# Optimization experiments

Measured on AMD Instinct MI355X. Metric: run time of the kernel, lower is better.

Reference implementation:

```python
import jax, jax.numpy as jnp
import numpy as np

EMBED = 1024
HEADS = 16
HEAD_DIM = EMBED // HEADS
T = 1024
B = 2
TEMP = 1.0
EPS = 1e-20


def setup_inputs() -> dict:
    key = jax.random.key(0)
    ks = jax.random.split(key, 8)
    s = 0.02  # xavier-ish init scale
    return {
        "g": jax.random.normal(ks[0], (T, B, EMBED), dtype=jnp.float32),
        "h": jax.random.normal(ks[1], (T, B, EMBED), dtype=jnp.float32),
        "g_in_w": jax.random.normal(ks[2], (3 * EMBED, EMBED), dtype=jnp.float32) * s,
        "g_in_b": jnp.zeros((3 * EMBED,), dtype=jnp.float32),
        "h_in_w": jax.random.normal(ks[3], (2 * EMBED, EMBED), dtype=jnp.float32) * s,
        "h_in_b": jnp.zeros((2 * EMBED,), dtype=jnp.float32),
        "g_out_w": jax.random.normal(ks[4], (EMBED, EMBED), dtype=jnp.float32) * s,
        "g_out_b": jnp.zeros((EMBED,), dtype=jnp.float32),
        "h_out_w": jax.random.normal(ks[5], (EMBED, EMBED), dtype=jnp.float32) * s,
        "h_out_b": jnp.zeros((EMBED,), dtype=jnp.float32),
    }


def reference(g, h, g_in_w, g_in_b, h_in_w, h_in_b, g_out_w, g_out_b, h_out_w, h_out_b):
    Tt, Bb, E = g.shape
    H, d = HEADS, HEAD_DIM

    # fused qkv projection on g stream, kv on h stream (F.linear: x @ W^T + b)
    q, gk, gv = jnp.split(g @ g_in_w.T + g_in_b, 3, axis=-1)
    hk, hv = jnp.split(h @ h_in_w.T + h_in_b, 2, axis=-1)
    q = q * (d ** -0.5)

    def to_heads(x):  # [T,B,E] -> [B,H,T,d]
        return x.reshape(Tt, Bb, H, d).transpose(1, 2, 0, 3)

    q, gk, gv, hk, hv = map(to_heads, (q, gk, gv, hk, hv))

    # dual-stream attention scores
    g_scores = jnp.einsum("bhtd,bhsd->bhts", q, gk)
    h_scores = jnp.einsum("bhtd,bhsd->bhts", q, hk)

    g_p = jax.nn.softmax(g_scores, axis=-1)
    h_p = jax.nn.softmax(h_scores, axis=-1)

    # gumbel-softmax sample of h_scores (mode='gumbel', temperature=TEMP)
    u = jax.random.uniform(jax.random.key(42), h_scores.shape, dtype=h_scores.dtype)
    noise = -jnp.log(-jnp.log(u + EPS) + EPS)
    sample = jax.nn.softmax((jax.nn.log_softmax(h_scores, axis=-1) + noise) / TEMP, axis=-1)

    g_attn = jnp.einsum("bhts,bhsd->bhtd", g_p, gv)
    h_attn = jnp.einsum("bhts,bhsd->bhtd", sample, hv)

    def merge(x):  # [B,H,T,d] -> [T,B,E]
        return x.transpose(2, 0, 1, 3).reshape(Tt, Bb, E)

    g_out = merge(g_attn) @ g_out_w.T + g_out_b
    h_out = merge(h_attn) @ h_out_w.T + h_out_b
    return g_out, h_out
```

## Files before the change

kernel.cpp:

```cpp
#include <hip/hip_runtime.h>
#include <stdint.h>

#define T_SEQ 1024

typedef __attribute__((ext_vector_type(8))) short short8;
typedef __attribute__((ext_vector_type(4))) float f32x4;
typedef __attribute__((ext_vector_type(4))) unsigned short ushort4v;
typedef __attribute__((ext_vector_type(8))) unsigned short ushort8v;

__device__ __forceinline__ unsigned short f2bf(float f) {
  union { float f; uint32_t u; } v; v.f = f;
  return (unsigned short)((v.u + 0x7fffu + ((v.u >> 16) & 1u)) >> 16);
}
__device__ __forceinline__ float bf2f(unsigned short u) {
  union { uint32_t u; float f; } v; v.u = ((uint32_t)u) << 16;
  return v.f;
}

__device__ __forceinline__ void gl2lds16(const unsigned short* g, unsigned short* l) {
  __builtin_amdgcn_global_load_lds(
      (const __attribute__((address_space(1))) void*)g,
      (__attribute__((address_space(3))) void*)l, 16, 0, 0);
}

__device__ __forceinline__ uint32_t tf_bits(uint32_t flat) {
  const uint32_t ks1 = 42u;
  const uint32_t ks2 = 0x1BD11BDAu ^ 42u;
  uint32_t x0 = 0u;
  uint32_t x1 = flat + ks1;
#define TFR(r) { x0 += x1; x1 = (x1 << (r)) | (x1 >> (32 - (r))); x1 ^= x0; }
  TFR(13) TFR(15) TFR(26) TFR(6)
  x0 += ks1; x1 += ks2 + 1u;
  TFR(17) TFR(29) TFR(16) TFR(24)
  x0 += ks2; x1 += 2u;
  TFR(13) TFR(15) TFR(26) TFR(6)
  x1 += ks1 + 3u;
  TFR(17) TFR(29) TFR(16) TFR(24)
  x0 += ks1; x1 += ks2 + 4u;
  TFR(13) TFR(15) TFR(26) TFR(6)
  x0 += ks2; x1 += 5u;
#undef TFR
  return x0 ^ x1;
}

__device__ __forceinline__ float gumbel_noise(uint32_t flat) {
  const uint32_t bits = tf_bits(flat);
  const float u = __uint_as_float((bits >> 9) | 0x3f800000u) - 1.0f;
  return -__logf(-__logf(u + 1e-20f) + 1e-20f);
}

__global__ __launch_bounds__(256) void convert_pre(
    const float* __restrict__ g, const float* __restrict__ h,
    const float* __restrict__ wgi_f, const float* __restrict__ whi_f,
    const float* __restrict__ wgo_f, const float* __restrict__ who_f,
    unsigned short* __restrict__ gbf, unsigned short* __restrict__ hbf,
    unsigned short* __restrict__ wgi, unsigned short* __restrict__ whi,
    unsigned short* __restrict__ wgo, unsigned short* __restrict__ who)
{
  const int64_t Q_SPLIT = 1048576;
  const int64_t Q_TOTAL = Q_SPLIT + 1835008;
  for (int64_t qd = (int64_t)blockIdx.x * 256 + threadIdx.x; qd < Q_TOTAL;
       qd += (int64_t)gridDim.x * 256) {
    if (qd < Q_SPLIT) {
      const int which = qd >= 524288;
      const int64_t e = (qd - (which ? 524288 : 0)) * 4;
      const float4 v = *(const float4*)((which ? h : g) + e);
      ushort4v u = {f2bf(v.x), f2bf(v.y), f2bf(v.z), f2bf(v.w)};
      *(ushort4v*)((which ? hbf : gbf) + e) = u;
    } else {
      int64_t off = qd - Q_SPLIT;
      const float* src; unsigned short* dst;
      if (off < 786432)                 { src = wgi_f; dst = wgi; }
      else if (off < 1310720)           { off -= 786432;  src = whi_f; dst = whi; }
      else if (off < 1572864)           { off -= 1310720; src = wgo_f; dst = wgo; }
      else                              { off -= 1572864; src = who_f; dst = who; }
      const int64_t e = off * 4;
      const float4 v = *(const float4*)(src + e);
      ushort4v u = {f2bf(v.x), f2bf(v.y), f2bf(v.z), f2bf(v.w)};
      *(ushort4v*)(dst + e) = u;
    }
  }
}

template<int TM, bool BF16OUT>
__device__ __forceinline__ void gemm_plain_core(
    const unsigned short* __restrict__ Ab, const unsigned short* __restrict__ Wb,
    const float* __restrict__ bias, int N, int K, int m0, int n0,
    int scale_limit, void* Cout, unsigned short* sA, unsigned short* sW)
{
  const int tid = threadIdx.x;
  const int w = tid >> 6;
  const int lane = tid & 63;
  const int txl = lane & 15, q = lane >> 4;
  const int wr = (w >> 1) * (TM * 16);
  const int wc = (w & 1) << 6;
  const int lr = lane >> 3, lu = lane & 7;
  const int rx7 = txl & 7;

  const unsigned short* Asrc = Ab + (size_t)(m0 + w * 8 * TM + lr) * K + ((lu ^ lr) << 3);
  const unsigned short* Wsrc = Wb + (size_t)(n0 + w * 32 + lr) * K + ((lu ^ lr) << 3);
  unsigned short* sAd = sA + (w * 8 * TM) * 64;
  unsigned short* sWd = sW + (w * 32) * 64;

  f32x4 acc[TM][4];
#pragma unroll
  for (int i = 0; i < TM; i++)
#pragma unroll
    for (int j = 0; j < 4; j++) acc[i][j] = (f32x4){0.f, 0.f, 0.f, 0.f};

  for (int k0 = 0; k0 < K; k0 += 64) {
    __syncthreads();
#pragma unroll
    for (int i = 0; i < TM; i++)
      gl2lds16(Asrc + (size_t)(8 * i) * K + k0, sAd + (8 * i) * 64);
#pragma unroll
    for (int i = 0; i < 4; i++)
      gl2lds16(Wsrc + (size_t)(8 * i) * K + k0, sWd + (8 * i) * 64);
    __syncthreads();
#pragma unroll
    for (int kk = 0; kk < 2; kk++) {
      const int uoff = ((4 * kk + q) ^ rx7) << 3;
      short8 af[TM], wf[4];
#pragma unroll
      for (int i = 0; i < TM; i++)
        af[i] = *(const short8*)&sA[(wr + 16 * i + txl) * 64 + uoff];
#pragma unroll
      for (int j = 0; j < 4; j++)
        wf[j] = *(const short8*)&sW[(wc + 16 * j + txl) * 64 + uoff];
#pragma unroll
      for (int i = 0; i < TM; i++)
#pragma unroll
        for (int j = 0; j < 4; j++)
          acc[i][j] = __builtin_amdgcn_mfma_f32_16x16x32_bf16(af[i], wf[j], acc[i][j], 0, 0, 0);
    }
  }

#pragma unroll
  for (int j = 0; j < 4; j++) {
    const int col = n0 + wc + 16 * j + txl;
    const float bj = bias[col];
    const float sc = (col < scale_limit) ? 0.125f : 1.0f;
#pragma unroll
    for (int i = 0; i < TM; i++) {
      const int rbase = m0 + wr + 16 * i + 4 * q;
#pragma unroll
      for (int r = 0; r < 4; r++) {
        const float v = (acc[i][j][r] + bj) * sc;
        if (BF16OUT) ((unsigned short*)Cout)[(size_t)(rbase + r) * N + col] = f2bf(v);
        else         ((float*)Cout)[(size_t)(rbase + r) * N + col] = v;
      }
    }
  }
}

__global__ __launch_bounds__(256, 4) void gemm_inproj(
    const unsigned short* __restrict__ gbf, const unsigned short* __restrict__ wgi,
    const float* __restrict__ bgi,
    const unsigned short* __restrict__ hbf, const unsigned short* __restrict__ whi,
    const float* __restrict__ bhi,
    unsigned short* __restrict__ qkv, unsigned short* __restrict__ hkv)
{
  __shared__ __align__(16) unsigned short sm[16384];
  const int bx = blockIdx.x;
  const int m0 = blockIdx.y * 128;
  if (bx < 24)
    gemm_plain_core<4, true>(gbf, wgi, bgi, 3072, 1024, m0, bx * 128, 1024,
                             qkv, sm, sm + 8192);
  else
    gemm_plain_core<4, true>(hbf, whi, bhi, 2048, 1024, m0, (bx - 24) * 128, 0,
                             hkv, sm, sm + 8192);
}

__global__ __launch_bounds__(256, 2) void gemm_outproj(
    const unsigned short* __restrict__ attnb,
    const unsigned short* __restrict__ wgo, const float* __restrict__ bgo,
    const unsigned short* __restrict__ who, const float* __restrict__ bho,
    float* __restrict__ out)
{
  __shared__ __align__(16) unsigned short sm[12288];
  const int m0 = blockIdx.y * 64;
  const unsigned short* Wp = (m0 < 2048) ? wgo : who;
  const float* bp = (m0 < 2048) ? bgo : bho;
  gemm_plain_core<2, false>(attnb, Wp, bp, 1024, 1024, m0, blockIdx.x * 128, 0,
                            out, sm, sm + 4096);
}

__global__ __launch_bounds__(256) void transpose_v(
    const unsigned short* __restrict__ qkv, const unsigned short* __restrict__ hkv,
    unsigned short* __restrict__ vTg, unsigned short* __restrict__ vTh)
{
  __shared__ __align__(16) unsigned short sm[64 * 72];
  const int tid = threadIdx.x;
  const int t0 = blockIdx.x * 64;
  const int d0 = blockIdx.y * 64;
  const int zb = blockIdx.z;
  const int b = zb & 1;
  const int strm = zb >> 1;
  const unsigned short* src = strm ? hkv : qkv;
  const int srcoff = strm ? 1024 : 2048;
  const int sstride = strm ? 2048 : 3072;
  unsigned short* dst = strm ? vTh : vTg;

  const int r = tid >> 2, cs = (tid & 3) << 4;
  {
    const size_t gsrc = (size_t)((t0 + r) * 2 + b) * sstride + srcoff + d0 + cs;
    *(ushort8v*)&sm[r * 72 + cs]     = *(const ushort8v*)&src[gsrc];
    *(ushort8v*)&sm[r * 72 + cs + 8] = *(const ushort8v*)&src[gsrc + 8];
  }
  __syncthreads();
  const int dr = tid >> 2, ts = (tid & 3) << 4;
  ushort8v o0, o1;
#pragma unroll
  for (int m = 0; m < 8; m++) o0[m] = sm[(ts + m) * 72 + dr];
#pragma unroll
  for (int m = 0; m < 8; m++) o1[m] = sm[(ts + 8 + m) * 72 + dr];
  const size_t gdst = (size_t)b * 1048576 + (size_t)(d0 + dr) * 1024 + t0 + ts;
  *(ushort8v*)&dst[gdst]     = o0;
  *(ushort8v*)&dst[gdst + 8] = o1;
}

__global__ __launch_bounds__(256, 4) void attn_mfma(
    const unsigned short* __restrict__ qkv, const unsigned short* __restrict__ hkv,
    const unsigned short* __restrict__ vTg, const unsigned short* __restrict__ vTh,
    float* __restrict__ Opart, float* __restrict__ lpart)
{
  __shared__ __align__(16) unsigned short smem[17408];
  unsigned short* KV = smem;
  unsigned short* PC = smem + 8192;
  unsigned short* QS = smem + 8192;

  const int tid = threadIdx.x;
  const int w = tid >> 6;
  const int lane = tid & 63;
  const int txl = lane & 15, q = lane >> 4;
  const int rx7 = txl & 7;
  const int lr = lane >> 3, lu = lane & 7;
  const int su = (lu ^ lr) << 3;
  const int t0 = blockIdx.x * 64;
  const int bh = blockIdx.y;
  const int z = blockIdx.z;
  const int b = bh >> 4;
  const int head = bh & 15;
  const int hoff = head * 64;
  const int sr = tid >> 2;
  const int sc = (tid & 3) << 4;

  {
    const size_t gq = ((size_t)(t0 + sr) * 2 + b) * 3072 + hoff + sc;
    *(ushort8v*)&QS[sr * 72 + sc]     = *(const ushort8v*)&qkv[gq];
    *(ushort8v*)&QS[sr * 72 + sc + 8] = *(const ushort8v*)&qkv[gq + 8];
  }
  __syncthreads();
  const short8 aq0 = *(const short8*)&QS[(16 * w + txl) * 72 + 8 * q];
  const short8 aq1 = *(const short8*)&QS[(16 * w + txl) * 72 + 32 + 8 * q];

  f32x4 Og[4], Oh[4];
  float l_g[4], l_h[4];
#pragma unroll
  for (int i = 0; i < 4; i++) {
    Og[i] = (f32x4){0.f, 0.f, 0.f, 0.f};
    Oh[i] = (f32x4){0.f, 0.f, 0.f, 0.f};
    l_g[i] = 0.f; l_h[i] = 0.f;
  }

  unsigned short* pcg = PC + (w * 2 + 0) * 1152;
  unsigned short* pch = PC + (w * 2 + 1) * 1152;

  const int s_begin = z * (T_SEQ / 2);
  const int s_end = s_begin + (T_SEQ / 2);
  for (int s0 = s_begin; s0 < s_end; s0 += 64) {
    __syncthreads();
#pragma unroll
    for (int t = 0; t < 2; t++) {
      const int srow = w * 16 + t * 8 + lr;
      const size_t grow = (size_t)(s0 + srow) * 2 + b;
      gl2lds16(&qkv[grow * 3072 + 1024 + hoff + su], &KV[(w * 16 + t * 8) * 64]);
      gl2lds16(&hkv[grow * 2048 +        hoff + su], &KV[4096 + (w * 16 + t * 8) * 64]);
    }
    float ng[4][4];
#pragma unroll
    for (int nt = 0; nt < 4; nt++)
#pragma unroll
      for (int r = 0; r < 4; r++) {
        const uint32_t trow = (uint32_t)(t0 + 16 * w + 4 * q + r);
        const uint32_t scol_ = (uint32_t)(s0 + 16 * nt + txl);
        ng[nt][r] = gumbel_noise(((uint32_t)bh << 20) | (trow << 10) | scol_);
      }
    __syncthreads();

    f32x4 Sg[4], Sh[4];
    const f32x4 zz = (f32x4){0.f, 0.f, 0.f, 0.f};
#pragma unroll
    for (int nt = 0; nt < 4; nt++) {
      const int srw = (16 * nt + txl) * 64;
      const int u0 = (q ^ rx7) << 3;
      const int u1 = ((4 + q) ^ rx7) << 3;
      const short8 bg0 = *(const short8*)&KV[srw + u0];
      const short8 bg1 = *(const short8*)&KV[srw + u1];
      const short8 bh0 = *(const short8*)&KV[4096 + srw + u0];
      const short8 bh1 = *(const short8*)&KV[4096 + srw + u1];
      f32x4 ag = __builtin_amdgcn_mfma_f32_16x16x32_bf16(aq0, bg0, zz, 0, 0, 0);
      ag = __builtin_amdgcn_mfma_f32_16x16x32_bf16(aq1, bg1, ag, 0, 0, 0);
      f32x4 ah = __builtin_amdgcn_mfma_f32_16x16x32_bf16(aq0, bh0, zz, 0, 0, 0);
      ah = __builtin_amdgcn_mfma_f32_16x16x32_bf16(aq1, bh1, ah, 0, 0, 0);
      Sg[nt] = ag; Sh[nt] = ah;
    }

#pragma unroll
    for (int nt = 0; nt < 4; nt++) {
      float eg[4], eh[4];
#pragma unroll
      for (int r = 0; r < 4; r++) {
        eg[r] = __expf(Sg[nt][r]);            l_g[r] += eg[r];
        eh[r] = __expf(Sh[nt][r] + ng[nt][r]); l_h[r] += eh[r];
      }
      const int sbase = (16 * nt + txl) * 18 + 4 * q;
      *(uint32_t*)&pcg[sbase]     = (uint32_t)f2bf(eg[0]) | ((uint32_t)f2bf(eg[1]) << 16);
      *(uint32_t*)&pcg[sbase + 2] = (uint32_t)f2bf(eg[2]) | ((uint32_t)f2bf(eg[3]) << 16);
      *(uint32_t*)&pch[sbase]     = (uint32_t)f2bf(eh[0]) | ((uint32_t)f2bf(eh[1]) << 16);
      *(uint32_t*)&pch[sbase + 2] = (uint32_t)f2bf(eh[2]) | ((uint32_t)f2bf(eh[3]) << 16);
    }

    __syncthreads();
#pragma unroll
    for (int t = 0; t < 2; t++) {
      const int drow = w * 16 + t * 8 + lr;
      const size_t gv = (size_t)b * 1048576 + (size_t)(hoff + drow) * 1024 + s0 + su;
      gl2lds16(&vTg[gv], &KV[(w * 16 + t * 8) * 64]);
      gl2lds16(&vTh[gv], &KV[4096 + (w * 16 + t * 8) * 64]);
    }
    short8 apg[2], aph[2];
#pragma unroll
    for (int c = 0; c < 2; c++)
#pragma unroll
      for (int j = 0; j < 8; j++) {
        apg[c][j] = (short)pcg[(32 * c + 8 * q + j) * 18 + txl];
        aph[c][j] = (short)pch[(32 * c + 8 * q + j) * 18 + txl];
      }
    __syncthreads();

#pragma unroll
    for (int c = 0; c < 2; c++) {
#pragma unroll
      for (int nt = 0; nt < 4; nt++) {
        const int drw = (16 * nt + txl) * 64;
        const int uv = (((4 * c + q) ^ rx7)) << 3;
        const short8 bvg = *(const short8*)&KV[drw + uv];
        const short8 bvh = *(const short8*)&KV[4096 + drw + uv];
        Og[nt] = __builtin_amdgcn_mfma_f32_16x16x32_bf16(apg[c], bvg, Og[nt], 0, 0, 0);
        Oh[nt] = __builtin_amdgcn_mfma_f32_16x16x32_bf16(aph[c], bvh, Oh[nt], 0, 0, 0);
      }
    }
  }

  float* opg = Opart + ((size_t)(z * 2 + 0) * 2048) * 1024;
  float* oph = Opart + ((size_t)(z * 2 + 1) * 2048) * 1024;
  float* lpg = lpart + (size_t)(z * 2 + 0) * 2048 * 16;
  float* lph = lpart + (size_t)(z * 2 + 1) * 2048 * 16;
#pragma unroll
  for (int r = 0; r < 4; r++) {
    float lg = l_g[r], lh = l_h[r];
    lg += __shfl_xor(lg, 1); lg += __shfl_xor(lg, 2);
    lg += __shfl_xor(lg, 4); lg += __shfl_xor(lg, 8);
    lh += __shfl_xor(lh, 1); lh += __shfl_xor(lh, 2);
    lh += __shfl_xor(lh, 4); lh += __shfl_xor(lh, 8);
    const int row = (t0 + 16 * w + 4 * q + r) * 2 + b;
    if (txl == 0) {
      lpg[row * 16 + head] = lg;
      lph[row * 16 + head] = lh;
    }
    const size_t base = (size_t)row * 1024 + hoff;
#pragma unroll
    for (int nt = 0; nt < 4; nt++) {
      opg[base + 16 * nt + txl] = Og[nt][r];
      oph[base + 16 * nt + txl] = Oh[nt][r];
    }
  }
}

__global__ __launch_bounds__(256) void merge_attn(
    const float* __restrict__ Opart, const float* __restrict__ lpart,
    unsigned short* __restrict__ attnb)
{
  const int idx = blockIdx.x * 256 + threadIdx.x;
  const int st = idx >> 19;
  const int i = idx & 0x7FFFF;
  const int row = i >> 8;
  const int colq = i & 255;
  const int head = colq >> 4;
  const float4 o0 = *(const float4*)&Opart[((size_t)(0 + st) * 2048 + row) * 1024 + colq * 4];
  const float4 o1 = *(const float4*)&Opart[((size_t)(2 + st) * 2048 + row) * 1024 + colq * 4];
  const float l0 = lpart[(size_t)(0 + st) * 32768 + row * 16 + head];
  const float l1 = lpart[(size_t)(2 + st) * 32768 + row * 16 + head];
  const float inv = 1.0f / (l0 + l1);
  ushort4v u = {f2bf((o0.x + o1.x) * inv), f2bf((o0.y + o1.y) * inv),
                f2bf((o0.z + o1.z) * inv), f2bf((o0.w + o1.w) * inv)};
  *(ushort4v*)&attnb[((size_t)st * 2048 + row) * 1024 + colq * 4] = u;
}

extern "C" void kernel_launch(void* const* d_in, const int* in_sizes, int n_in,
                              void* d_out, int out_size, void* d_ws, size_t ws_size,
                              hipStream_t stream) {
  const float* g       = (const float*)d_in[0];
  const float* h       = (const float*)d_in[1];
  const float* g_in_w  = (const float*)d_in[2];
  const float* g_in_b  = (const float*)d_in[3];
  const float* h_in_w  = (const float*)d_in[4];
  const float* h_in_b  = (const float*)d_in[5];
  const float* g_out_w = (const float*)d_in[6];
  const float* g_out_b = (const float*)d_in[7];
  const float* h_out_w = (const float*)d_in[8];
  const float* h_out_b = (const float*)d_in[9];
  float* out = (float*)d_out;

  unsigned short* ws = (unsigned short*)d_ws;
  unsigned short* qkv   = ws;
  unsigned short* hkv   = qkv + (size_t)2048*3072;
  unsigned short* attnb = hkv + (size_t)2048*2048;
  unsigned short* wgo   = attnb + (size_t)4096*1024;
  unsigned short* who   = wgo + (size_t)1024*1024;
  unsigned short* scratch = who + (size_t)1024*1024;
  unsigned short* gbf = scratch;
  unsigned short* hbf = gbf + (size_t)2048*1024;
  unsigned short* wgi = hbf + (size_t)2048*1024;
  unsigned short* whi = wgi + (size_t)3072*1024;
  float* Opart = (float*)scratch;
  float* lpart = Opart + (size_t)4*2048*1024;
  unsigned short* vTg = (unsigned short*)(lpart + (size_t)4*2048*16);
  unsigned short* vTh = vTg + (size_t)2*1024*1024;

  convert_pre<<<1024, 256, 0, stream>>>(g, h, g_in_w, h_in_w, g_out_w, h_out_w,
                                        gbf, hbf, wgi, whi, wgo, who);
  gemm_inproj<<<dim3(40, 16), 256, 0, stream>>>(
      gbf, wgi, g_in_b, hbf, whi, h_in_b, qkv, hkv);
  transpose_v<<<dim3(16, 16, 4), 256, 0, stream>>>(qkv, hkv, vTg, vTh);
  attn_mfma<<<dim3(T_SEQ / 64, 32, 2), 256, 0, stream>>>(qkv, hkv, vTg, vTh, Opart, lpart);
  merge_attn<<<4096, 256, 0, stream>>>(Opart, lpart, attnb);
  gemm_outproj<<<dim3(8, 64), 256, 0, stream>>>(
      attnb, wgo, g_out_b, who, h_out_b, out);
}
```

Before: 278.1 us.

## Shrink attention key tile to 32, load K and V together, raise occupancy

```diff
diff --git a/kernel.cpp b/kernel.cpp
--- a/kernel.cpp
+++ b/kernel.cpp
@@ -219,15 +219,16 @@
   *(ushort8v*)&dst[gdst + 8] = o1;
 }
 
-__global__ __launch_bounds__(256, 4) void attn_mfma(
+__global__ __launch_bounds__(256, 6) void attn_mfma(
     const unsigned short* __restrict__ qkv, const unsigned short* __restrict__ hkv,
     const unsigned short* __restrict__ vTg, const unsigned short* __restrict__ vTh,
     float* __restrict__ Opart, float* __restrict__ lpart)
 {
-  __shared__ __align__(16) unsigned short smem[17408];
-  unsigned short* KV = smem;
+  __shared__ __align__(16) unsigned short smem[12800];
+  unsigned short* KB = smem;
+  unsigned short* VB = smem + 4096;
   unsigned short* PC = smem + 8192;
-  unsigned short* QS = smem + 8192;
+  unsigned short* QS = smem;
 
   const int tid = threadIdx.x;
   const int w = tid >> 6;
@@ -236,6 +237,8 @@
   const int rx7 = txl & 7;
   const int lr = lane >> 3, lu = lane & 7;
   const int su = (lu ^ lr) << 3;
+  const int lg_ = lu ^ lr;
+  const int vsig = lg_ >> 2, vm = lg_ & 3;
   const int t0 = blockIdx.x * 64;
   const int bh = blockIdx.y;
   const int z = blockIdx.z;
@@ -263,23 +266,27 @@
     l_g[i] = 0.f; l_h[i] = 0.f;
   }
 
-  unsigned short* pcg = PC + (w * 2 + 0) * 1152;
-  unsigned short* pch = PC + (w * 2 + 1) * 1152;
+  unsigned short* pcg = PC + (w * 2 + 0) * 576;
+  unsigned short* pch = PC + (w * 2 + 1) * 576;
+  const unsigned short* vsrc = (vsig ? vTh : vTg) + (size_t)b * 1048576;
 
   const int s_begin = z * (T_SEQ / 2);
   const int s_end = s_begin + (T_SEQ / 2);
-  for (int s0 = s_begin; s0 < s_end; s0 += 64) {
+  for (int s0 = s_begin; s0 < s_end; s0 += 32) {
     __syncthreads();
+    {
+      const size_t krow = (size_t)(s0 + w * 8 + lr) * 2 + b;
+      gl2lds16(&qkv[krow * 3072 + 1024 + hoff + su], &KB[(w * 8) * 64]);
+      gl2lds16(&hkv[krow * 2048 +        hoff + su], &KB[2048 + (w * 8) * 64]);
+    }
 #pragma unroll
     for (int t = 0; t < 2; t++) {
-      const int srow = w * 16 + t * 8 + lr;
-      const size_t grow = (size_t)(s0 + srow) * 2 + b;
-      gl2lds16(&qkv[grow * 3072 + 1024 + hoff + su], &KV[(w * 16 + t * 8) * 64]);
-      gl2lds16(&hkv[grow * 2048 +        hoff + su], &KV[4096 + (w * 16 + t * 8) * 64]);
-    }
-    float ng[4][4];
-#pragma unroll
-    for (int nt = 0; nt < 4; nt++)
+      const int rb = w * 16 + 8 * t;
+      gl2lds16(&vsrc[(size_t)(hoff + rb + lr) * 1024 + s0 + 8 * vm], &VB[rb * 64]);
+    }
+    float ng[2][4];
+#pragma unroll
+    for (int nt = 0; nt < 2; nt++)
 #pragma unroll
       for (int r = 0; r < 4; r++) {
         const uint32_t trow = (uint32_t)(t0 + 16 * w + 4 * q + r);
@@ -288,30 +295,32 @@
       }
     __syncthreads();
 
-    f32x4 Sg[4], Sh[4];
+    f32x4 Sg[2], Sh[2];
     const f32x4 zz = (f32x4){0.f, 0.f, 0.f, 0.f};
-#pragma unroll
-    for (int nt = 0; nt < 4; nt++) {
+    const int u0 = (q ^ rx7) << 3;
+    const int u1 = ((4 + q) ^ rx7) << 3;
+    __builtin_amdgcn_s_setprio(1);
+#pragma unroll
+    for (int nt = 0; nt < 2; nt++) {
       const int srw = (16 * nt + txl) * 64;
-      const int u0 = (q ^ rx7) << 3;
-      const int u1 = ((4 + q) ^ rx7) << 3;
-      const short8 bg0 = *(const short8*)&KV[srw + u0];
-      const short8 bg1 = *(const short8*)&KV[srw + u1];
-      const short8 bh0 = *(const short8*)&KV[4096 + srw + u0];
-      const short8 bh1 = *(const short8*)&KV[4096 + srw + u1];
+      const short8 bg0 = *(const short8*)&KB[srw + u0];
+      const short8 bg1 = *(const short8*)&KB[srw + u1];
+      const short8 bh0 = *(const short8*)&KB[2048 + srw + u0];
+      const short8 bh1 = *(const short8*)&KB[2048 + srw + u1];
       f32x4 ag = __builtin_amdgcn_mfma_f32_16x16x32_bf16(aq0, bg0, zz, 0, 0, 0);
       ag = __builtin_amdgcn_mfma_f32_16x16x32_bf16(aq1, bg1, ag, 0, 0, 0);
       f32x4 ah = __builtin_amdgcn_mfma_f32_16x16x32_bf16(aq0, bh0, zz, 0, 0, 0);
       ah = __builtin_amdgcn_mfma_f32_16x16x32_bf16(aq1, bh1, ah, 0, 0, 0);
       Sg[nt] = ag; Sh[nt] = ah;
     }
-
-#pragma unroll
-    for (int nt = 0; nt < 4; nt++) {
+    __builtin_amdgcn_s_setprio(0);
+
+#pragma unroll
+    for (int nt = 0; nt < 2; nt++) {
       float eg[4], eh[4];
 #pragma unroll
       for (int r = 0; r < 4; r++) {
-        eg[r] = __expf(Sg[nt][r]);            l_g[r] += eg[r];
+        eg[r] = __expf(Sg[nt][r]);             l_g[r] += eg[r];
         eh[r] = __expf(Sh[nt][r] + ng[nt][r]); l_h[r] += eh[r];
       }
       const int sbase = (16 * nt + txl) * 18 + 4 * q;
@@ -321,36 +330,23 @@
       *(uint32_t*)&pch[sbase + 2] = (uint32_t)f2bf(eh[2]) | ((uint32_t)f2bf(eh[3]) << 16);
     }
 
-    __syncthreads();
-#pragma unroll
-    for (int t = 0; t < 2; t++) {
-      const int drow = w * 16 + t * 8 + lr;
-      const size_t gv = (size_t)b * 1048576 + (size_t)(hoff + drow) * 1024 + s0 + su;
-      gl2lds16(&vTg[gv], &KV[(w * 16 + t * 8) * 64]);
-      gl2lds16(&vTh[gv], &KV[4096 + (w * 16 + t * 8) * 64]);
-    }
-    short8 apg[2], aph[2];
-#pragma unroll
-    for (int c = 0; c < 2; c++)
-#pragma unroll
-      for (int j = 0; j < 8; j++) {
-        apg[c][j] = (short)pcg[(32 * c + 8 * q + j) * 18 + txl];
-        aph[c][j] = (short)pch[(32 * c + 8 * q + j) * 18 + txl];
-      }
-    __syncthreads();
-
-#pragma unroll
-    for (int c = 0; c < 2; c++) {
-#pragma unroll
-      for (int nt = 0; nt < 4; nt++) {
-        const int drw = (16 * nt + txl) * 64;
-        const int uv = (((4 * c + q) ^ rx7)) << 3;
-        const short8 bvg = *(const short8*)&KV[drw + uv];
-        const short8 bvh = *(const short8*)&KV[4096 + drw + uv];
-        Og[nt] = __builtin_amdgcn_mfma_f32_16x16x32_bf16(apg[c], bvg, Og[nt], 0, 0, 0);
-        Oh[nt] = __builtin_amdgcn_mfma_f32_16x16x32_bf16(aph[c], bvh, Oh[nt], 0, 0, 0);
-      }
-    }
+    short8 apg, aph;
+#pragma unroll
+    for (int j = 0; j < 8; j++) {
+      apg[j] = (short)pcg[(8 * q + j) * 18 + txl];
+      aph[j] = (short)pch[(8 * q + j) * 18 + txl];
+    }
+
+    __builtin_amdgcn_s_setprio(1);
+#pragma unroll
+    for (int nt = 0; nt < 4; nt++) {
+      const int drw = (16 * nt + txl) * 64;
+      const short8 bvg = *(const short8*)&VB[drw + u0];
+      const short8 bvh = *(const short8*)&VB[drw + u1];
+      Og[nt] = __builtin_amdgcn_mfma_f32_16x16x32_bf16(apg, bvg, Og[nt], 0, 0, 0);
+      Oh[nt] = __builtin_amdgcn_mfma_f32_16x16x32_bf16(aph, bvh, Oh[nt], 0, 0, 0);
+    }
+    __builtin_amdgcn_s_setprio(0);
   }
 
   float* opg = Opart + ((size_t)(z * 2 + 0) * 2048) * 1024;
```

New measurement: 309.1 us. +11.2%, slower.

## Load K and V tiles together into separate LDS buffers, drop mid-loop barriers

Applied to the files above, without the earlier changes.

```diff
diff --git a/kernel.cpp b/kernel.cpp
--- a/kernel.cpp
+++ b/kernel.cpp
@@ -219,15 +219,16 @@
   *(ushort8v*)&dst[gdst + 8] = o1;
 }
 
-__global__ __launch_bounds__(256, 4) void attn_mfma(
+__global__ __launch_bounds__(256, 3) void attn_mfma(
     const unsigned short* __restrict__ qkv, const unsigned short* __restrict__ hkv,
     const unsigned short* __restrict__ vTg, const unsigned short* __restrict__ vTh,
     float* __restrict__ Opart, float* __restrict__ lpart)
 {
-  __shared__ __align__(16) unsigned short smem[17408];
-  unsigned short* KV = smem;
-  unsigned short* PC = smem + 8192;
-  unsigned short* QS = smem + 8192;
+  __shared__ __align__(16) unsigned short smem[25600];
+  unsigned short* KB = smem;
+  unsigned short* VB = smem + 8192;
+  unsigned short* PC = smem + 16384;
+  unsigned short* QS = smem;
 
   const int tid = threadIdx.x;
   const int w = tid >> 6;
@@ -265,6 +266,12 @@
 
   unsigned short* pcg = PC + (w * 2 + 0) * 1152;
   unsigned short* pch = PC + (w * 2 + 1) * 1152;
+  const unsigned short* vTgb = vTg + (size_t)b * 1048576;
+  const unsigned short* vThb = vTh + (size_t)b * 1048576;
+
+  const int u0 = (q ^ rx7) << 3;
+  const int u1 = ((4 + q) ^ rx7) << 3;
+  const f32x4 zz = (f32x4){0.f, 0.f, 0.f, 0.f};
 
   const int s_begin = z * (T_SEQ / 2);
   const int s_end = s_begin + (T_SEQ / 2);
@@ -272,10 +279,13 @@
     __syncthreads();
 #pragma unroll
     for (int t = 0; t < 2; t++) {
-      const int srow = w * 16 + t * 8 + lr;
-      const size_t grow = (size_t)(s0 + srow) * 2 + b;
-      gl2lds16(&qkv[grow * 3072 + 1024 + hoff + su], &KV[(w * 16 + t * 8) * 64]);
-      gl2lds16(&hkv[grow * 2048 +        hoff + su], &KV[4096 + (w * 16 + t * 8) * 64]);
+      const int rb = w * 16 + 8 * t;
+      const size_t krow = (size_t)(s0 + rb + lr) * 2 + b;
+      gl2lds16(&qkv[krow * 3072 + 1024 + hoff + su], &KB[rb * 64]);
+      gl2lds16(&hkv[krow * 2048 +        hoff + su], &KB[4096 + rb * 64]);
+      const size_t vrow = (size_t)(hoff + rb + lr) * 1024 + s0 + su;
+      gl2lds16(&vTgb[vrow], &VB[rb * 64]);
+      gl2lds16(&vThb[vrow], &VB[4096 + rb * 64]);
     }
     float ng[4][4];
 #pragma unroll
@@ -289,29 +299,28 @@
     __syncthreads();
 
     f32x4 Sg[4], Sh[4];
-    const f32x4 zz = (f32x4){0.f, 0.f, 0.f, 0.f};
+    __builtin_amdgcn_s_setprio(1);
 #pragma unroll
     for (int nt = 0; nt < 4; nt++) {
       const int srw = (16 * nt + txl) * 64;
-      const int u0 = (q ^ rx7) << 3;
-      const int u1 = ((4 + q) ^ rx7) << 3;
-      const short8 bg0 = *(const short8*)&KV[srw + u0];
-      const short8 bg1 = *(const short8*)&KV[srw + u1];
-      const short8 bh0 = *(const short8*)&KV[4096 + srw + u0];
-      const short8 bh1 = *(const short8*)&KV[4096 + srw + u1];
+      const short8 bg0 = *(const short8*)&KB[srw + u0];
+      const short8 bg1 = *(const short8*)&KB[srw + u1];
+      const short8 bh0 = *(const short8*)&KB[4096 + srw + u0];
+      const short8 bh1 = *(const short8*)&KB[4096 + srw + u1];
       f32x4 ag = __builtin_amdgcn_mfma_f32_16x16x32_bf16(aq0, bg0, zz, 0, 0, 0);
       ag = __builtin_amdgcn_mfma_f32_16x16x32_bf16(aq1, bg1, ag, 0, 0, 0);
       f32x4 ah = __builtin_amdgcn_mfma_f32_16x16x32_bf16(aq0, bh0, zz, 0, 0, 0);
       ah = __builtin_amdgcn_mfma_f32_16x16x32_bf16(aq1, bh1, ah, 0, 0, 0);
       Sg[nt] = ag; Sh[nt] = ah;
     }
+    __builtin_amdgcn_s_setprio(0);
 
 #pragma unroll
     for (int nt = 0; nt < 4; nt++) {
       float eg[4], eh[4];
 #pragma unroll
       for (int r = 0; r < 4; r++) {
-        eg[r] = __expf(Sg[nt][r]);            l_g[r] += eg[r];
+        eg[r] = __expf(Sg[nt][r]);             l_g[r] += eg[r];
         eh[r] = __expf(Sh[nt][r] + ng[nt][r]); l_h[r] += eh[r];
       }
       const int sbase = (16 * nt + txl) * 18 + 4 * q;
@@ -321,14 +330,6 @@
       *(uint32_t*)&pch[sbase + 2] = (uint32_t)f2bf(eh[2]) | ((uint32_t)f2bf(eh[3]) << 16);
     }
 
-    __syncthreads();
-#pragma unroll
-    for (int t = 0; t < 2; t++) {
-      const int drow = w * 16 + t * 8 + lr;
-      const size_t gv = (size_t)b * 1048576 + (size_t)(hoff + drow) * 1024 + s0 + su;
-      gl2lds16(&vTg[gv], &KV[(w * 16 + t * 8) * 64]);
-      gl2lds16(&vTh[gv], &KV[4096 + (w * 16 + t * 8) * 64]);
-    }
     short8 apg[2], aph[2];
 #pragma unroll
     for (int c = 0; c < 2; c++)
@@ -337,20 +338,21 @@
         apg[c][j] = (short)pcg[(32 * c + 8 * q + j) * 18 + txl];
         aph[c][j] = (short)pch[(32 * c + 8 * q + j) * 18 + txl];
       }
-    __syncthreads();
-
+
+    __builtin_amdgcn_s_setprio(1);
 #pragma unroll
     for (int c = 0; c < 2; c++) {
+      const int uv = (c == 0) ? u0 : u1;
 #pragma unroll
       for (int nt = 0; nt < 4; nt++) {
         const int drw = (16 * nt + txl) * 64;
-        const int uv = (((4 * c + q) ^ rx7)) << 3;
-        const short8 bvg = *(const short8*)&KV[drw + uv];
-        const short8 bvh = *(const short8*)&KV[4096 + drw + uv];
+        const short8 bvg = *(const short8*)&VB[drw + uv];
+        const short8 bvh = *(const short8*)&VB[4096 + drw + uv];
         Og[nt] = __builtin_amdgcn_mfma_f32_16x16x32_bf16(apg[c], bvg, Og[nt], 0, 0, 0);
         Oh[nt] = __builtin_amdgcn_mfma_f32_16x16x32_bf16(aph[c], bvh, Oh[nt], 0, 0, 0);
       }
     }
+    __builtin_amdgcn_s_setprio(0);
   }
 
   float* opg = Opart + ((size_t)(z * 2 + 0) * 2048) * 1024;
```

Result: faster. 267.2 us (-3.9%).
